# Performance work log

Hardware: AMD Instinct MI355X
Metric: run time of the kernel (lower is better)

## Reference

```python
import jax, jax.numpy as jnp
import numpy as np

D_MODEL = 1024
N_HEADS = 16
D_K = D_MODEL // N_HEADS
SEQ = 2048
BATCH = 2
THETA = 10000.0


def _rope(x, token_positions):
    # x: [b, h, s, dk]; token_positions: [s] int
    k = jnp.arange(0, D_K, 2, dtype=jnp.float32)
    freqs = 1.0 / (THETA ** (k / D_K))                    # [dk/2]
    angles = token_positions.astype(jnp.float32)[:, None] * freqs[None, :]  # [s, dk/2]
    cos = jnp.cos(angles)
    sin = jnp.sin(angles)
    x1 = x[..., 0::2]
    x2 = x[..., 1::2]
    r1 = x1 * cos - x2 * sin
    r2 = x1 * sin + x2 * cos
    out = jnp.stack([r1, r2], axis=-1)                    # [b,h,s,dk/2,2]
    return out.reshape(x.shape)


def setup_inputs() -> dict:
    key = jax.random.key(0)
    ks = jax.random.split(key, 5)
    sigma = np.sqrt(2.0 / (D_MODEL + D_MODEL))
    x = jax.random.normal(ks[0], (BATCH, SEQ, D_MODEL), dtype=jnp.float32)
    Wq = jax.random.truncated_normal(ks[1], -3.0, 3.0, (D_MODEL, D_MODEL), dtype=jnp.float32) * sigma
    Wk = jax.random.truncated_normal(ks[2], -3.0, 3.0, (D_MODEL, D_MODEL), dtype=jnp.float32) * sigma
    Wv = jax.random.truncated_normal(ks[3], -3.0, 3.0, (D_MODEL, D_MODEL), dtype=jnp.float32) * sigma
    Wo = jax.random.truncated_normal(ks[4], -3.0, 3.0, (D_MODEL, D_MODEL), dtype=jnp.float32) * sigma
    token_positions = jnp.arange(SEQ, dtype=jnp.int64)
    return {"x": x, "Wq": Wq, "Wk": Wk, "Wv": Wv, "Wo": Wo, "token_positions": token_positions}


def reference(x, Wq, Wk, Wv, Wo, token_positions):
    b, s, d = x.shape
    # projections: Linear stores weight [out,in], applies x @ W.T
    Q = x @ Wq.T
    K = x @ Wk.T
    V = x @ Wv.T
    # [b, s, h*dk] -> [b, h, s, dk]
    def split_heads(t):
        return t.reshape(b, s, N_HEADS, D_K).transpose(0, 2, 1, 3)
    Q, K, V = split_heads(Q), split_heads(K), split_heads(V)
    Q = _rope(Q, token_positions)
    K = _rope(K, token_positions)
    scale = 1.0 / np.sqrt(D_K).astype(np.float32)
    scores = jnp.einsum('bhqd,bhkd->bhqk', Q, K) * scale   # [b,h,s,s]
    causal = jnp.tril(jnp.ones((s, s), dtype=bool))
    scores = jnp.where(causal, scores, -jnp.inf)
    attn = jax.nn.softmax(scores, axis=-1)
    out = jnp.einsum('bhqk,bhkd->bhqd', attn, V)           # [b,h,s,dk]
    out = out.transpose(0, 2, 1, 3).reshape(b, s, d)
    return out @ Wo.T
```

## Files before the change

kernel.cpp:

```cpp
#include <hip/hip_runtime.h>
#include <hip/hip_bf16.h>
#include <stdint.h>

#define SEQL   2048
#define NBATCH 2
#define BSZ    4096
#define DMODEL 1024
#define NH     16
#define DK     64
#define NBH    32
#define NCHUNK_TOT 40

typedef __attribute__((ext_vector_type(8)))  short short8;
typedef __attribute__((ext_vector_type(4)))  short shortx4;
typedef __attribute__((ext_vector_type(4)))  float f32x4;
typedef __attribute__((ext_vector_type(16))) float f32x16;
typedef __attribute__((ext_vector_type(4)))  unsigned uint4v;
union PU { uint4v u; short8 s; };

__device__ __forceinline__ short f2b(float f) {
  unsigned u = __float_as_uint(f);
  u = (u + 0x7FFF + ((u >> 16) & 1)) >> 16;
  return (short)u;
}
__device__ __forceinline__ float b2f(short s) {
  return __uint_as_float(((unsigned)(unsigned short)s) << 16);
}
__device__ __forceinline__ unsigned cvtpk(float lo, float hi) {
  unsigned r;
  asm("v_cvt_pk_bf16_f32 %0, %1, %2" : "=v"(r) : "v"(lo), "v"(hi));
  return r;
}
#define PLSWAP(a_, b_) asm("v_permlane32_swap_b32 %0, %1" : "+v"(a_), "+v"(b_))

__device__ __forceinline__ void g2l16(const void* g, void* l) {
  __builtin_amdgcn_global_load_lds(
      (__attribute__((address_space(1))) void*)(uintptr_t)g,
      (__attribute__((address_space(3))) void*)l, 16, 0, 0);
}

__device__ __forceinline__ f32x4 mfma16(short8 a, short8 b, f32x4 c) {
  return __builtin_amdgcn_mfma_f32_16x16x32_bf16(a, b, c, 0, 0, 0);
}
__device__ __forceinline__ f32x16 mfma32(short8 a, short8 b, f32x16 c) {
  return __builtin_amdgcn_mfma_f32_32x32x16_bf16(a, b, c, 0, 0, 0);
}

__global__ void cvt_all(const float* __restrict__ x,  const float* __restrict__ wq,
                        const float* __restrict__ wk, const float* __restrict__ wv,
                        const float* __restrict__ wo, short* __restrict__ xb,
                        short* __restrict__ wqkv, short* __restrict__ wob) {
  long idx = ((long)blockIdx.x * 256 + threadIdx.x) * 4;
  const float* s; short* d; long off;
  if (idx < 4194304L)      { s = x;  d = xb;             off = idx; }
  else if (idx < 5242880L) { s = wq; d = wqkv;           off = idx - 4194304L; }
  else if (idx < 6291456L) { s = wk; d = wqkv + 1048576; off = idx - 5242880L; }
  else if (idx < 7340032L) { s = wv; d = wqkv + 2097152; off = idx - 6291456L; }
  else                     { s = wo; d = wob;            off = idx - 7340032L; }
  float4 v = *(const float4*)(s + off);
  shortx4 r;
  r[0] = f2b(v.x); r[1] = f2b(v.y); r[2] = f2b(v.z); r[3] = f2b(v.w);
  *(shortx4*)(d + off) = r;
}

template<int CBF16>
__global__ __launch_bounds__(256, 2)
void gemm_bt(const short* __restrict__ A, const short* __restrict__ B,
             void* __restrict__ Cv, int M, int N, int K,
             long bStride, long cStride) {
  __shared__ short As[4096];
  __shared__ short Bs[4096];
  B += (long)blockIdx.y * bStride;
  int nbn = N >> 7;
  int bm = blockIdx.x / nbn, bn = blockIdx.x % nbn;
  int tid = threadIdx.x, w = tid >> 6, l = tid & 63;
  int wm = w >> 1, wn = w & 1;
  int lr = l & 15, lg = l >> 4;
  int brow = bm << 7, bcol = bn << 7;

  const f32x4 fz = {0.f, 0.f, 0.f, 0.f};
  f32x4 acc[4][4];
#pragma unroll
  for (int xi = 0; xi < 4; ++xi)
#pragma unroll
    for (int yi = 0; yi < 4; ++yi) acc[xi][yi] = fz;

  for (int k0 = 0; k0 < K; k0 += 32) {
#pragma unroll
    for (int i = 0; i < 2; ++i) {
      int c = w * 2 + i;
      int chunk = c * 64 + l;
      int row = chunk >> 2, ch = chunk & 3;
      int gch = ch ^ ((row >> 1) & 3);
      g2l16(A + (long)(brow + row) * K + k0 + gch * 8, &As[c * 512]);
      g2l16(B + (long)(bcol + row) * K + k0 + gch * 8, &Bs[c * 512]);
    }
    __syncthreads();

    short8 af[4], bf[4];
#pragma unroll
    for (int xi = 0; xi < 4; ++xi) {
      int ar = wm * 64 + xi * 16 + lr;
      af[xi] = *(const short8*)&As[ar * 32 + ((lg ^ ((ar >> 1) & 3)) << 3)];
      int br = wn * 64 + xi * 16 + lr;
      bf[xi] = *(const short8*)&Bs[br * 32 + ((lg ^ ((br >> 1) & 3)) << 3)];
    }
#pragma unroll
    for (int xi = 0; xi < 4; ++xi)
#pragma unroll
      for (int yi = 0; yi < 4; ++yi)
        acc[xi][yi] = mfma16(af[xi], bf[yi], acc[xi][yi]);
    __syncthreads();
  }

  if (CBF16) {
    short* C = (short*)Cv + (long)blockIdx.y * cStride;
#pragma unroll
    for (int xi = 0; xi < 4; ++xi)
#pragma unroll
      for (int yi = 0; yi < 4; ++yi)
#pragma unroll
        for (int r = 0; r < 4; ++r) {
          int row = brow + wm * 64 + xi * 16 + lg * 4 + r;
          int col = bcol + wn * 64 + yi * 16 + lr;
          C[(long)row * N + col] = f2b(acc[xi][yi][r]);
        }
  } else {
    float* C = (float*)Cv;
#pragma unroll
    for (int xi = 0; xi < 4; ++xi)
#pragma unroll
      for (int yi = 0; yi < 4; ++yi)
#pragma unroll
        for (int r = 0; r < 4; ++r) {
          int row = brow + wm * 64 + xi * 16 + lg * 4 + r;
          int col = bcol + wn * 64 + yi * 16 + lr;
          C[(long)row * N + col] = acc[xi][yi][r];
        }
  }
}

__global__ void rope_split(const short* __restrict__ qkv, const int* __restrict__ tok,
                           short* __restrict__ Qh, short* __restrict__ Kh) {
  int t = blockIdx.x * 256 + threadIdx.x;
  int qd = t & 15, h = (t >> 4) & 15, bs = t >> 8;
  int b = bs >> 11, s = bs & 2047;
  float pos = (float)tok[s];
  long srcoff = (long)bs * 1024 + h * 64 + qd * 4;
  shortx4 q4 = *(const shortx4*)(qkv + srcoff);
  shortx4 k4 = *(const shortx4*)(qkv + 4194304L + srcoff);
  shortx4 qo, ko;
#pragma unroll
  for (int p = 0; p < 2; ++p) {
    int i = qd * 2 + p;
    float freq = exp2f(-(float)i * (13.287712379549449f / 32.0f));
    float ang = pos * freq;
    float sn, cs;
    sincosf(ang, &sn, &cs);
    const float QS = 0.125f * 1.44269504f;
    float x1 = b2f(q4[p * 2]), x2 = b2f(q4[p * 2 + 1]);
    qo[p * 2]     = f2b((x1 * cs - x2 * sn) * QS);
    qo[p * 2 + 1] = f2b((x1 * sn + x2 * cs) * QS);
    float y1 = b2f(k4[p * 2]), y2 = b2f(k4[p * 2 + 1]);
    ko[p * 2]     = f2b(y1 * cs - y2 * sn);
    ko[p * 2 + 1] = f2b(y1 * sn + y2 * cs);
  }
  long outoff = ((long)(b * 16 + h) * 2048 + s) * 64 + qd * 4;
  *(shortx4*)(Qh + outoff) = qo;
  *(shortx4*)(Kh + outoff) = ko;
}

__global__ void vtrans(const short* __restrict__ Vlin, short* __restrict__ Vt) {
  __shared__ short tile[64][72];
  int s0 = blockIdx.x * 64;
  int bh = blockIdx.y;
  int b = bh >> 4, h = bh & 15;
  int t = threadIdx.x;
  int r = t >> 2, c0 = (t & 3) * 16;
  const short* src = Vlin + ((long)(b * 2048 + s0 + r)) * 1024 + h * 64 + c0;
  *(short8*)&tile[r][c0]     = *(const short8*)src;
  *(short8*)&tile[r][c0 + 8] = *(const short8*)(src + 8);
  __syncthreads();
  int d = t >> 2, sc0 = (t & 3) * 16;
  short8 o0, o1;
#pragma unroll
  for (int j = 0; j < 8; ++j) { o0[j] = tile[sc0 + j][d]; o1[j] = tile[sc0 + 8 + j][d]; }
  short* dst = Vt + ((long)(bh * 64 + d)) * 2048 + s0 + sc0;
  *(short8*)dst       = o0;
  *(short8*)(dst + 8) = o1;
}

__global__ __launch_bounds__(256, 3)
void attn_fwd(const short* __restrict__ Qh, const short* __restrict__ Kh,
              const short* __restrict__ Vt, short* __restrict__ poO,
              float* __restrict__ pmb, float* __restrict__ plb) {
  __shared__ short Ks[3][4096];
  __shared__ short Vs[3][4096];
  int bh = blockIdx.x;
  int xr = 39 - blockIdx.y;
  int qi, c = xr, nc = 1;
  for (qi = 0; qi < 16; ++qi) { nc = (qi >> 2) + 1; if (c < nc) break; c -= nc; }
  int n = 2 * qi + 2;
  int t0 = (c * n) / nc, t1 = ((c + 1) * n) / nc;
  int q0b = qi << 7;
  int tid = threadIdx.x, w = tid >> 6, l = tid & 63;
  int ql = l & 31, hi = l >> 5;
  const short* Qb = Qh + (long)bh * (2048 * 64);
  const short* Kb = Kh + (long)bh * (2048 * 64);
  const short* Vb = Vt + (long)bh * (64 * 2048);
  int qw = q0b + 32 * w;
  int qg = qw + ql;
  int pid = bh * NCHUNK_TOT + xr;

  short8 qf[4];
#pragma unroll
  for (int kc = 0; kc < 4; ++kc)
    qf[kc] = *(const short8*)(Qb + (long)qg * 64 + kc * 16 + hi * 8);

  f32x16 o0, o1;
#pragma unroll
  for (int r = 0; r < 16; ++r) { o0[r] = 0.f; o1[r] = 0.f; }
  float m = -1e30f, lsum = 0.f;

#define STAGE(t_, bufi_) do {                                                   \
    int s0_ = (t_) << 6;                                                        \
    _Pragma("unroll")                                                           \
    for (int i_ = 0; i_ < 2; ++i_) {                                            \
      int c_ = w + 4 * i_;                                                      \
      int g_ = c_ >> 2, cc_ = c_ & 3;                                           \
      g2l16(Kb + ((long)(s0_ + g_ * 32 + ql)) * 64 + cc_ * 16 + hi * 8,         \
            &Ks[bufi_][c_ * 512]);                                              \
      g2l16(Vb + ((long)(g_ * 32 + ql)) * 2048 + s0_ + cc_ * 16 + hi * 8,       \
            &Vs[bufi_][c_ * 512]);                                              \
    }                                                                           \
  } while (0)

  STAGE(t0, 0);
  if (t0 + 1 < t1) STAGE(t0 + 1, 1);
  int cur = 0;

  for (int t = t0; t < t1; ++t) {
    if (t + 2 < t1) {
      int nb = cur + 2; if (nb >= 3) nb -= 3;
      STAGE(t + 2, nb);
      asm volatile("s_waitcnt vmcnt(8)" ::: "memory");
    } else if (t + 1 < t1) {
      asm volatile("s_waitcnt vmcnt(4)" ::: "memory");
    } else {
      asm volatile("s_waitcnt vmcnt(0)" ::: "memory");
    }
    __builtin_amdgcn_s_barrier();
    int s0 = t << 6;
    if (s0 <= qw + 31) {
      bool upper = (s0 + 32 <= qw + 31);
      f32x16 sT0, sT1;
#pragma unroll
      for (int r = 0; r < 16; ++r) { sT0[r] = 0.f; sT1[r] = 0.f; }
      __builtin_amdgcn_s_setprio(1);
#pragma unroll
      for (int kc = 0; kc < 4; ++kc) {
        short8 k0 = *(const short8*)&Ks[cur][(kc * 64 + l) * 8];
        sT0 = mfma32(k0, qf[kc], sT0);
      }
      if (upper) {
#pragma unroll
        for (int kc = 0; kc < 4; ++kc) {
          short8 k1 = *(const short8*)&Ks[cur][((4 + kc) * 64 + l) * 8];
          sT1 = mfma32(k1, qf[kc], sT1);
        }
      }
      __builtin_amdgcn_s_setprio(0);
      if (s0 + 63 > qw) {
#pragma unroll
        for (int r = 0; r < 16; ++r) {
          int kvl = (r & 3) + 8 * (r >> 2) + 4 * hi;
          if (s0 + kvl > qg) sT0[r] = -1e30f;
        }
        if (upper) {
#pragma unroll
          for (int r = 0; r < 16; ++r) {
            int kvl = (r & 3) + 8 * (r >> 2) + 4 * hi;
            if (s0 + 32 + kvl > qg) sT1[r] = -1e30f;
          }
        }
      }
      float pmax = sT0[0];
#pragma unroll
      for (int r = 1; r < 16; ++r) pmax = fmaxf(pmax, sT0[r]);
      if (upper) {
#pragma unroll
        for (int r = 0; r < 16; ++r) pmax = fmaxf(pmax, sT1[r]);
      }
      pmax = fmaxf(pmax, __shfl_xor(pmax, 32));
      if (__any(pmax > m + 11.5416f)) {
        float mn = fmaxf(m, pmax);
        float sf = exp2f(m - mn);
        m = mn;
        lsum *= sf;
#pragma unroll
        for (int r = 0; r < 16; ++r) {
          int row = (r & 3) + 8 * (r >> 2) + 4 * hi;
          float fo = __shfl(sf, row);
          o0[r] *= fo; o1[r] *= fo;
        }
      }
      float rs = 0.f;
#pragma unroll
      for (int r = 0; r < 16; ++r) {
        float p = exp2f(sT0[r] - m);
        sT0[r] = p; rs += p;
      }
      if (upper) {
#pragma unroll
        for (int r = 0; r < 16; ++r) {
          float p = exp2f(sT1[r] - m);
          sT1[r] = p; rs += p;
        }
      }
      rs += __shfl_xor(rs, 32);
      lsum += rs;
      short8 pa[4];
      {
        unsigned cA[4], cB[4];
#pragma unroll
        for (int g = 0; g < 4; ++g) {
          cA[g] = cvtpk(sT0[4 * g], sT0[4 * g + 1]);
          cB[g] = cvtpk(sT0[4 * g + 2], sT0[4 * g + 3]);
        }
        PLSWAP(cA[0], cA[1]); PLSWAP(cB[0], cB[1]);
        PLSWAP(cA[2], cA[3]); PLSWAP(cB[2], cB[3]);
        PU p0; p0.u = (uint4v){cA[0], cB[0], cA[1], cB[1]}; pa[0] = p0.s;
        PU p1; p1.u = (uint4v){cA[2], cB[2], cA[3], cB[3]}; pa[1] = p1.s;
      }
      if (upper) {
        unsigned cA[4], cB[4];
#pragma unroll
        for (int g = 0; g < 4; ++g) {
          cA[g] = cvtpk(sT1[4 * g], sT1[4 * g + 1]);
          cB[g] = cvtpk(sT1[4 * g + 2], sT1[4 * g + 3]);
        }
        PLSWAP(cA[0], cA[1]); PLSWAP(cB[0], cB[1]);
        PLSWAP(cA[2], cA[3]); PLSWAP(cB[2], cB[3]);
        PU p2; p2.u = (uint4v){cA[0], cB[0], cA[1], cB[1]}; pa[2] = p2.s;
        PU p3; p3.u = (uint4v){cA[2], cB[2], cA[3], cB[3]}; pa[3] = p3.s;
      }
      __builtin_amdgcn_s_setprio(1);
#pragma unroll
      for (int kc = 0; kc < 2; ++kc) {
        short8 v0 = *(const short8*)&Vs[cur][(kc * 64 + l) * 8];
        short8 v1 = *(const short8*)&Vs[cur][((4 + kc) * 64 + l) * 8];
        o0 = mfma32(pa[kc], v0, o0);
        o1 = mfma32(pa[kc], v1, o1);
      }
      if (upper) {
#pragma unroll
        for (int kc = 2; kc < 4; ++kc) {
          short8 v0 = *(const short8*)&Vs[cur][(kc * 64 + l) * 8];
          short8 v1 = *(const short8*)&Vs[cur][((4 + kc) * 64 + l) * 8];
          o0 = mfma32(pa[kc], v0, o0);
          o1 = mfma32(pa[kc], v1, o1);
        }
      }
      __builtin_amdgcn_s_setprio(0);
    }
    asm volatile("s_waitcnt lgkmcnt(0)" ::: "memory");
    __builtin_amdgcn_s_barrier();
    ++cur; if (cur >= 3) cur -= 3;
  }
#undef STAGE

  if (hi == 0) {
    pmb[pid * 128 + w * 32 + ql] = m;
    plb[pid * 128 + w * 32 + ql] = lsum;
  }
#pragma unroll
  for (int r = 0; r < 16; ++r) {
    int row = (r & 3) + 8 * (r >> 2) + 4 * hi;
    long basep = ((long)pid * 128 + w * 32 + row) * 64;
    poO[basep + ql]      = f2b(o0[r]);
    poO[basep + 32 + ql] = f2b(o1[r]);
  }
}

__global__ void attn_combine(const short* __restrict__ poO,
                             const float* __restrict__ pmb,
                             const float* __restrict__ plb,
                             short* __restrict__ Oh) {
  int x = blockIdx.x, bh = blockIdx.y;
  int qi = x >> 2, sub = x & 3;
  int t = threadIdx.x;
  int r = sub * 32 + (t >> 3);
  int d0 = (t & 7) * 8;
  int nc = (qi >> 2) + 1;
  int prefix = 0;
  for (int j = 0; j < qi; ++j) prefix += (j >> 2) + 1;
  int base = bh * NCHUNK_TOT + prefix;
  float M = -1e30f;
  for (int i = 0; i < nc; ++i)
    M = fmaxf(M, pmb[(base + i) * 128 + r]);
  float acc0 = 0, acc1 = 0, acc2 = 0, acc3 = 0, acc4 = 0, acc5 = 0, acc6 = 0, acc7 = 0;
  float den = 0.f;
  for (int i = 0; i < nc; ++i) {
    float wgt = exp2f(pmb[(base + i) * 128 + r] - M);
    den += wgt * plb[(base + i) * 128 + r];
    short8 ov = *(const short8*)&poO[((long)(base + i) * 128 + r) * 64 + d0];
    acc0 += wgt * b2f(ov[0]); acc1 += wgt * b2f(ov[1]);
    acc2 += wgt * b2f(ov[2]); acc3 += wgt * b2f(ov[3]);
    acc4 += wgt * b2f(ov[4]); acc5 += wgt * b2f(ov[5]);
    acc6 += wgt * b2f(ov[6]); acc7 += wgt * b2f(ov[7]);
  }
  float inv = 1.0f / den;
  int b = bh >> 4, h = bh & 15;
  int s = qi * 128 + r;
  short8 out;
  out[0] = f2b(acc0 * inv); out[1] = f2b(acc1 * inv);
  out[2] = f2b(acc2 * inv); out[3] = f2b(acc3 * inv);
  out[4] = f2b(acc4 * inv); out[5] = f2b(acc5 * inv);
  out[6] = f2b(acc6 * inv); out[7] = f2b(acc7 * inv);
  *(short8*)&Oh[((long)(b * 2048 + s)) * 1024 + h * 64 + d0] = out;
}

extern "C" void kernel_launch(void* const* d_in, const int* in_sizes, int n_in,
                              void* d_out, int out_size, void* d_ws, size_t ws_size,
                              hipStream_t stream) {
  const float* x  = (const float*)d_in[0];
  const float* wq = (const float*)d_in[1];
  const float* wk = (const float*)d_in[2];
  const float* wv = (const float*)d_in[3];
  const float* wo = (const float*)d_in[4];
  const int* tok  = (const int*)d_in[5];

  short* wsp  = (short*)d_ws;
  short* xb   = wsp;
  short* wqkv = xb + 4194304;
  short* wob  = wqkv + 3145728;
  short* qkv  = wob + 1048576;
  short* qh   = qkv + 12582912;
  short* kh   = qh + 4194304;
  short* vt   = kh + 4194304;
  short* oh   = vt + 4194304;

  short* poO = qkv;
  float* pmb = (float*)xb;
  float* plb = pmb + NCHUNK_TOT * NBH * 128;

  (void)in_sizes; (void)n_in; (void)out_size; (void)ws_size;

  cvt_all<<<8192, 256, 0, stream>>>(x, wq, wk, wv, wo, xb, wqkv, wob);
  gemm_bt<1><<<dim3(256, 3), 256, 0, stream>>>(xb, wqkv, qkv, 4096, 1024, 1024,
                                               1048576L, 4194304L);
  rope_split<<<4096, 256, 0, stream>>>(qkv, tok, qh, kh);
  vtrans<<<dim3(32, 32), 256, 0, stream>>>(qkv + 8388608, vt);
  attn_fwd<<<dim3(32, NCHUNK_TOT), 256, 0, stream>>>(qh, kh, vt, poO, pmb, plb);
  attn_combine<<<dim3(64, 32), 256, 0, stream>>>(poO, pmb, plb, oh);
  gemm_bt<0><<<dim3(256, 1), 256, 0, stream>>>(oh, wob, d_out, 4096, 1024, 1024,
                                               0L, 0L);
}
```

Baseline: 130.5 us.

## Use 256x256-tile pipelined GEMM for QKV projection and double-buffer output GEMM

```diff
diff --git a/kernel.cpp b/kernel.cpp
--- a/kernel.cpp
+++ b/kernel.cpp
@@ -63,13 +63,145 @@
   *(shortx4*)(d + off) = r;
 }
 
+__global__ __launch_bounds__(512, 1)
+void gemm256(const short* __restrict__ A, const short* __restrict__ B,
+             short* __restrict__ C) {
+  __shared__ short As[2][2][8192];
+  __shared__ short Bs[2][2][8192];
+  int id = blockIdx.x;
+  int swz = (id & 7) * 24 + (id >> 3);
+  int bm = swz / 12, bn = swz % 12;
+  int brow = bm << 8, bcol = bn << 8;
+  int tid = threadIdx.x, w = tid >> 6, l = tid & 63;
+  int wm = w >> 2, wn = w & 3;
+  int lr = l & 15, lg = l >> 4;
+  const short* Abase = A + (long)brow * 1024;
+  const short* Bbase = B + (long)bcol * 1024;
+
+  f32x4 acc[8][4];
+#pragma unroll
+  for (int mi = 0; mi < 8; ++mi)
+#pragma unroll
+    for (int ni = 0; ni < 4; ++ni) acc[mi][ni] = (f32x4){0.f, 0.f, 0.f, 0.f};
+
+#define STGH(srcbase_, kt_, dst_) do {                                          \
+    _Pragma("unroll")                                                           \
+    for (int i_ = 0; i_ < 2; ++i_) {                                            \
+      int idx_ = i_ * 512 + tid;                                                \
+      int r_ = idx_ >> 3, gch_ = (idx_ & 7) ^ (r_ & 7);                         \
+      g2l16((srcbase_) + (long)r_ * 1024 + (kt_) * 64 + gch_ * 8,               \
+            &(dst_)[idx_ * 8]);                                                 \
+    } } while (0)
+
+  STGH(Abase,          0, As[0][0]); STGH(Abase + 131072, 0, As[0][1]);
+  STGH(Bbase,          0, Bs[0][0]); STGH(Bbase + 131072, 0, Bs[0][1]);
+  STGH(Abase,          1, As[1][0]); STGH(Abase + 131072, 1, As[1][1]);
+  STGH(Bbase,          1, Bs[1][0]); STGH(Bbase + 131072, 1, Bs[1][1]);
+  asm volatile("s_waitcnt vmcnt(8)" ::: "memory");
+  __builtin_amdgcn_s_barrier();
+
+  int brw = (wn & 1) * 64;
+  for (int kt = 0; kt < 16; ++kt) {
+    int cur = kt & 1;
+    const short* Ah = &As[cur][wm][0];
+    const short* Bh = &Bs[cur][wn >> 1][0];
+    short8 a0[4][2], a1[4][2], bf[4][2];
+#pragma unroll
+    for (int mi = 0; mi < 4; ++mi)
+#pragma unroll
+      for (int ks = 0; ks < 2; ++ks)
+        a0[mi][ks] = *(const short8*)
+            &Ah[(mi * 16 + lr) * 64 + (((ks * 4 + lg) ^ (lr & 7)) << 3)];
+#pragma unroll
+    for (int ni = 0; ni < 4; ++ni)
+#pragma unroll
+      for (int ks = 0; ks < 2; ++ks)
+        bf[ni][ks] = *(const short8*)
+            &Bh[(brw + ni * 16 + lr) * 64 + (((ks * 4 + lg) ^ (lr & 7)) << 3)];
+    asm volatile("s_waitcnt lgkmcnt(0)" ::: "memory");
+    __builtin_amdgcn_sched_barrier(0);
+    __builtin_amdgcn_s_setprio(1);
+#pragma unroll
+    for (int mi = 0; mi < 4; ++mi)
+#pragma unroll
+      for (int ni = 0; ni < 2; ++ni)
+#pragma unroll
+        for (int ks = 0; ks < 2; ++ks)
+          acc[mi][ni] = mfma16(a0[mi][ks], bf[ni][ks], acc[mi][ni]);
+    __builtin_amdgcn_s_setprio(0);
+    __builtin_amdgcn_s_barrier();
+#pragma unroll
+    for (int mi = 0; mi < 4; ++mi)
+#pragma unroll
+      for (int ks = 0; ks < 2; ++ks)
+        a1[mi][ks] = *(const short8*)
+            &Ah[((mi + 4) * 16 + lr) * 64 + (((ks * 4 + lg) ^ (lr & 7)) << 3)];
+    __builtin_amdgcn_s_setprio(1);
+#pragma unroll
+    for (int mi = 0; mi < 4; ++mi)
+#pragma unroll
+      for (int ni = 2; ni < 4; ++ni)
+#pragma unroll
+        for (int ks = 0; ks < 2; ++ks)
+          acc[mi][ni] = mfma16(a0[mi][ks], bf[ni][ks], acc[mi][ni]);
+    __builtin_amdgcn_s_setprio(0);
+    asm volatile("s_waitcnt lgkmcnt(0)" ::: "memory");
+    __builtin_amdgcn_s_barrier();
+    if (kt + 2 < 16) {
+      STGH(Abase,          kt + 2, As[cur][0]);
+      STGH(Abase + 131072, kt + 2, As[cur][1]);
+    }
+    __builtin_amdgcn_s_setprio(1);
+#pragma unroll
+    for (int mi = 0; mi < 4; ++mi)
+#pragma unroll
+      for (int ni = 0; ni < 2; ++ni)
+#pragma unroll
+        for (int ks = 0; ks < 2; ++ks)
+          acc[mi + 4][ni] = mfma16(a1[mi][ks], bf[ni][ks], acc[mi + 4][ni]);
+    __builtin_amdgcn_s_setprio(0);
+    __builtin_amdgcn_s_barrier();
+    if (kt + 2 < 16) {
+      STGH(Bbase,          kt + 2, Bs[cur][0]);
+      STGH(Bbase + 131072, kt + 2, Bs[cur][1]);
+    }
+    __builtin_amdgcn_s_setprio(1);
+#pragma unroll
+    for (int mi = 0; mi < 4; ++mi)
+#pragma unroll
+      for (int ni = 2; ni < 4; ++ni)
+#pragma unroll
+        for (int ks = 0; ks < 2; ++ks)
+          acc[mi + 4][ni] = mfma16(a1[mi][ks], bf[ni][ks], acc[mi + 4][ni]);
+    __builtin_amdgcn_s_setprio(0);
+    if (kt + 1 < 16) {
+      if (kt + 2 < 16) asm volatile("s_waitcnt vmcnt(8)" ::: "memory");
+      else             asm volatile("s_waitcnt vmcnt(0)" ::: "memory");
+    }
+    __builtin_amdgcn_s_barrier();
+  }
+#undef STGH
+
+#pragma unroll
+  for (int mi = 0; mi < 8; ++mi)
+#pragma unroll
+    for (int ni = 0; ni < 4; ++ni)
+#pragma unroll
+      for (int rr = 0; rr < 4; ++rr) {
+        int grow = brow + wm * 128 + mi * 16 + lg * 4 + rr;
+        int gcol = bcol + wn * 64 + ni * 16 + lr;
+        int mat = gcol >> 10, cin = gcol & 1023;
+        C[(long)mat * 4194304 + (long)grow * 1024 + cin] = f2b(acc[mi][ni][rr]);
+      }
+}
+
 template<int CBF16>
 __global__ __launch_bounds__(256, 2)
 void gemm_bt(const short* __restrict__ A, const short* __restrict__ B,
              void* __restrict__ Cv, int M, int N, int K,
              long bStride, long cStride) {
-  __shared__ short As[4096];
-  __shared__ short Bs[4096];
+  __shared__ short As[2][4096];
+  __shared__ short Bs[2][4096];
   B += (long)blockIdx.y * bStride;
   int nbn = N >> 7;
   int bm = blockIdx.x / nbn, bn = blockIdx.x % nbn;
@@ -85,36 +217,51 @@
 #pragma unroll
     for (int yi = 0; yi < 4; ++yi) acc[xi][yi] = fz;
 
+#define GSTAGE(k0_, bi_) do {                                                   \
+    _Pragma("unroll")                                                           \
+    for (int i_ = 0; i_ < 2; ++i_) {                                            \
+      int c_ = w * 2 + i_;                                                      \
+      int chunk_ = c_ * 64 + l;                                                 \
+      int row_ = chunk_ >> 2, ch_ = chunk_ & 3;                                 \
+      int gch_ = ch_ ^ ((row_ >> 1) & 3);                                       \
+      g2l16(A + (long)(brow + row_) * K + (k0_) + gch_ * 8, &As[bi_][c_ * 512]);\
+      g2l16(B + (long)(bcol + row_) * K + (k0_) + gch_ * 8, &Bs[bi_][c_ * 512]);\
+    }                                                                           \
+  } while (0)
+
+  GSTAGE(0, 0);
   for (int k0 = 0; k0 < K; k0 += 32) {
-#pragma unroll
-    for (int i = 0; i < 2; ++i) {
-      int c = w * 2 + i;
-      int chunk = c * 64 + l;
-      int row = chunk >> 2, ch = chunk & 3;
-      int gch = ch ^ ((row >> 1) & 3);
-      g2l16(A + (long)(brow + row) * K + k0 + gch * 8, &As[c * 512]);
-      g2l16(B + (long)(bcol + row) * K + k0 + gch * 8, &Bs[c * 512]);
+    int cb = (k0 >> 5) & 1;
+    if (k0 + 32 < K) {
+      GSTAGE(k0 + 32, cb ^ 1);
+      asm volatile("s_waitcnt vmcnt(4)" ::: "memory");
+    } else {
+      asm volatile("s_waitcnt vmcnt(0)" ::: "memory");
     }
-    __syncthreads();
-
-    short8 af[4], bf[4];
+    __builtin_amdgcn_s_barrier();
+
+    short8 af[4], bfr[4];
 #pragma unroll
     for (int xi = 0; xi < 4; ++xi) {
       int ar = wm * 64 + xi * 16 + lr;
-      af[xi] = *(const short8*)&As[ar * 32 + ((lg ^ ((ar >> 1) & 3)) << 3)];
+      af[xi] = *(const short8*)&As[cb][ar * 32 + ((lg ^ ((ar >> 1) & 3)) << 3)];
       int br = wn * 64 + xi * 16 + lr;
-      bf[xi] = *(const short8*)&Bs[br * 32 + ((lg ^ ((br >> 1) & 3)) << 3)];
+      bfr[xi] = *(const short8*)&Bs[cb][br * 32 + ((lg ^ ((br >> 1) & 3)) << 3)];
     }
+    __builtin_amdgcn_s_setprio(1);
 #pragma unroll
     for (int xi = 0; xi < 4; ++xi)
 #pragma unroll
       for (int yi = 0; yi < 4; ++yi)
-        acc[xi][yi] = mfma16(af[xi], bf[yi], acc[xi][yi]);
-    __syncthreads();
-  }
+        acc[xi][yi] = mfma16(af[xi], bfr[yi], acc[xi][yi]);
+    __builtin_amdgcn_s_setprio(0);
+    asm volatile("s_waitcnt lgkmcnt(0)" ::: "memory");
+    __builtin_amdgcn_s_barrier();
+  }
+#undef GSTAGE
 
   if (CBF16) {
-    short* C = (short*)Cv + (long)blockIdx.y * cStride;
+    short* Cp = (short*)Cv + (long)blockIdx.y * cStride;
 #pragma unroll
     for (int xi = 0; xi < 4; ++xi)
 #pragma unroll
@@ -123,10 +270,10 @@
         for (int r = 0; r < 4; ++r) {
           int row = brow + wm * 64 + xi * 16 + lg * 4 + r;
           int col = bcol + wn * 64 + yi * 16 + lr;
-          C[(long)row * N + col] = f2b(acc[xi][yi][r]);
+          Cp[(long)row * N + col] = f2b(acc[xi][yi][r]);
         }
   } else {
-    float* C = (float*)Cv;
+    float* Cp = (float*)Cv;
 #pragma unroll
     for (int xi = 0; xi < 4; ++xi)
 #pragma unroll
@@ -135,7 +282,7 @@
         for (int r = 0; r < 4; ++r) {
           int row = brow + wm * 64 + xi * 16 + lg * 4 + r;
           int col = bcol + wn * 64 + yi * 16 + lr;
-          C[(long)row * N + col] = acc[xi][yi][r];
+          Cp[(long)row * N + col] = acc[xi][yi][r];
         }
   }
 }
@@ -447,8 +594,7 @@
   (void)in_sizes; (void)n_in; (void)out_size; (void)ws_size;
 
   cvt_all<<<8192, 256, 0, stream>>>(x, wq, wk, wv, wo, xb, wqkv, wob);
-  gemm_bt<1><<<dim3(256, 3), 256, 0, stream>>>(xb, wqkv, qkv, 4096, 1024, 1024,
-                                               1048576L, 4194304L);
+  gemm256<<<192, 512, 0, stream>>>(xb, wqkv, qkv);
   rope_split<<<4096, 256, 0, stream>>>(qkv, tok, qh, kh);
   vtrans<<<dim3(32, 32), 256, 0, stream>>>(qkv + 8388608, vt);
   attn_fwd<<<dim3(32, NCHUNK_TOT), 256, 0, stream>>>(qh, kh, vt, poO, pmb, plb);
```

Result: no change. 132.7 us (+1.7%).
